# Performance work log

Hardware: AMD Instinct MI355X
Metric: run time of the kernel (lower is better)

## Reference

```python
import jax, jax.numpy as jnp
import numpy as np

N_NODES = 50000
N_EDGES = 600000
N_RELS = 19
D_IN = 128
D_HID = 64
D_OUT = 2


def setup_inputs() -> dict:
    key = jax.random.key(0)
    ks = jax.random.split(key, 10)
    feat = jax.random.normal(ks[0], (N_NODES, D_IN), dtype=jnp.float32)
    src = jax.random.randint(ks[1], (N_EDGES,), 0, N_NODES)
    dst = jax.random.randint(ks[2], (N_EDGES,), 0, N_NODES)
    etype = jax.random.randint(ks[3], (N_EDGES,), 0, N_RELS)
    s1 = 1.0 / np.sqrt(D_IN)
    s2 = 1.0 / np.sqrt(D_HID)
    W1 = jax.random.normal(ks[4], (N_RELS, D_IN, D_HID), dtype=jnp.float32) * s1
    loop1 = jax.random.normal(ks[5], (D_IN, D_HID), dtype=jnp.float32) * s1
    b1 = jnp.zeros((D_HID,), dtype=jnp.float32)
    W2 = jax.random.normal(ks[6], (N_RELS, D_HID, D_OUT), dtype=jnp.float32) * s2
    loop2 = jax.random.normal(ks[7], (D_HID, D_OUT), dtype=jnp.float32) * s2
    b2 = jnp.zeros((D_OUT,), dtype=jnp.float32)
    return {"feat": feat, "W1": W1, "loop1": loop1, "b1": b1,
            "W2": W2, "loop2": loop2, "b2": b2,
            "src": src, "dst": dst, "etype": etype}


def _rel_graph_conv(h, W, loop_w, bias, src, dst, etype, activation):
    # Per-relation transform of all nodes: [N, R, O]; then gather per edge.
    # (num_rels * out_feat is small, so this is cheaper than gathering W per edge.)
    transformed = jnp.einsum('nd,rdo->nro', h, W)
    msg = transformed[src, etype]                      # [E, O] edge messages
    agg = jax.ops.segment_sum(msg, dst, num_segments=h.shape[0])  # scatter-add
    out = agg + h @ loop_w + bias                      # self-loop + bias
    if activation is not None:
        out = activation(out)
    return out


def reference(feat, W1, loop1, b1, W2, loop2, b2, src, dst, etype):
    h = _rel_graph_conv(feat, W1, loop1, b1, src, dst, etype, jax.nn.relu)
    h = _rel_graph_conv(h, W2, loop2, b2, src, dst, etype, None)
    return h
```

## Files before the change

kernel.cpp:

```cpp
#include <hip/hip_runtime.h>

#define N_NODES 50000
#define N_EDGES 600000
#define N_RELS  19
#define D_IN    128
#define D_HID   64
#define D_OUT   2

typedef unsigned short u16;
typedef unsigned int   u32;
typedef __attribute__((ext_vector_type(8))) short sfrag;
typedef __attribute__((ext_vector_type(4))) float f32x4;

__device__ __forceinline__ u16 f2bf(float f){
  union { float f; u32 i; } v; v.f = f;
  u32 r = v.i + 0x7fffu + ((v.i >> 16) & 1u);
  return (u16)(r >> 16);
}
__device__ __forceinline__ float bf2f(u16 u){
  union { u32 i; float f; } v; v.i = ((u32)u) << 16; return v.f;
}

__global__ __launch_bounds__(256) void k_featb(const float* __restrict__ feat,
                                               u16* __restrict__ featb){
  int i = blockIdx.x * 256 + threadIdx.x;
  float2 f = ((const float2*)feat)[i];
  ((u32*)featb)[i] = (u32)f2bf(f.x) | ((u32)f2bf(f.y) << 16);
}

__global__ void k_prep(const float* __restrict__ W1, const float* __restrict__ loop1,
                       const float* __restrict__ W2,
                       u16* __restrict__ W1Tb, u16* __restrict__ loop1Tb,
                       u16* __restrict__ W2Tb){
  int idx = blockIdx.x * 256 + threadIdx.x;
  const int T1 = N_RELS * D_HID * D_IN;
  const int T2 = T1 + N_RELS * 16 * D_HID;
  const int T3 = T2 + D_HID * D_IN;
  if (idx < T1) {
    int r = idx / (D_HID * D_IN);
    int t = idx - r * (D_HID * D_IN);
    int j = t >> 7, d = t & 127;
    W1Tb[idx] = f2bf(W1[(r * D_IN + d) * D_HID + j]);
  } else if (idx < T2) {
    int k2 = idx - T1;
    int r = k2 / (16 * D_HID);
    int t = k2 - r * (16 * D_HID);
    int n = t >> 6, k = t & 63;
    W2Tb[k2] = (n < D_OUT) ? f2bf(W2[(r * D_HID + k) * D_OUT + n]) : (u16)0;
  } else if (idx < T3) {
    int k2 = idx - T2;
    int j = k2 >> 7, d = k2 & 127;
    loop1Tb[k2] = f2bf(loop1[d * D_HID + j]);
  }
}

__global__ void k_zero(int* __restrict__ hist){
  if (threadIdx.x < N_RELS) hist[threadIdx.x] = 0;
}

__global__ __launch_bounds__(256) void k_hist(const int* __restrict__ et, int* __restrict__ hist){
  __shared__ int lh[N_RELS];
  int tid = threadIdx.x;
  if (tid < N_RELS) lh[tid] = 0;
  __syncthreads();
  int e = blockIdx.x * 256 + tid;
  if (e < N_EDGES) atomicAdd(&lh[et[e]], 1);
  __syncthreads();
  if (tid < N_RELS && lh[tid]) atomicAdd(&hist[tid], lh[tid]);
}

__global__ void k_scan(const int* __restrict__ hist, int* __restrict__ offs,
                       int* __restrict__ toff, int* __restrict__ cursor){
  if (threadIdx.x == 0) {
    int acc = 0, tacc = 0;
    offs[0] = 0; toff[0] = 0;
    for (int r = 0; r < N_RELS; ++r) {
      cursor[r] = acc;
      int c = hist[r];
      acc += c;               offs[r + 1] = acc;
      tacc += (c + 63) >> 6;  toff[r + 1] = tacc;
    }
  }
}

__global__ __launch_bounds__(256) void k_scatter(const int* __restrict__ et,
                                                 int* __restrict__ cursor,
                                                 int* __restrict__ perm){
  __shared__ int lh[N_RELS], base[N_RELS];
  int tid = threadIdx.x;
  if (tid < N_RELS) lh[tid] = 0;
  __syncthreads();
  int e = blockIdx.x * 256 + tid;
  int r = 0, my = 0;
  bool valid = e < N_EDGES;
  if (valid) { r = et[e]; my = atomicAdd(&lh[r], 1); }
  __syncthreads();
  if (tid < N_RELS && lh[tid]) base[tid] = atomicAdd(&cursor[tid], lh[tid]);
  __syncthreads();
  if (valid) perm[base[r] + my] = e;
}

__global__ __launch_bounds__(256) void k_selfloop1_mfma(
    const u16* __restrict__ featb, const u16* __restrict__ loop1Tb,
    const float* __restrict__ b1, u16* __restrict__ agg1b){
  __shared__ __align__(16) u16 Als[64][136];
  __shared__ __align__(16) u16 Bls[64][136];
  int tid = threadIdx.x;
  int base = blockIdx.x * 64;
  {
    int j = tid >> 2, seg = tid & 3;
    const uint4* g = (const uint4*)(loop1Tb + j * 128) + seg * 4;
    uint4* d = (uint4*)&Bls[j][seg * 32];
    d[0] = g[0]; d[1] = g[1]; d[2] = g[2]; d[3] = g[3];
  }
  {
    int i = tid >> 2, seg = tid & 3;
    int n = base + i; if (n >= N_NODES) n = N_NODES - 1;
    const uint4* g = (const uint4*)(featb + n * D_IN) + seg * 4;
    uint4* d = (uint4*)&Als[i][seg * 32];
    d[0] = g[0]; d[1] = g[1]; d[2] = g[2]; d[3] = g[3];
  }
  __syncthreads();

  int w = tid >> 6, lane = tid & 63;
  int r16 = lane & 15, c4 = lane >> 4;
  sfrag aF[4];
  #pragma unroll
  for (int kk = 0; kk < 4; ++kk)
    aF[kk] = *(const sfrag*)&Als[w * 16 + r16][kk * 32 + c4 * 8];
  #pragma unroll
  for (int ct = 0; ct < 4; ++ct) {
    f32x4 acc = {0.f, 0.f, 0.f, 0.f};
    #pragma unroll
    for (int kk = 0; kk < 4; ++kk) {
      sfrag bF = *(const sfrag*)&Bls[ct * 16 + r16][kk * 32 + c4 * 8];
      acc = __builtin_amdgcn_mfma_f32_16x16x32_bf16(aF[kk], bF, acc, 0, 0, 0);
    }
    int col = ct * 16 + r16;
    float bias = b1[col];
    #pragma unroll
    for (int reg = 0; reg < 4; ++reg) {
      int row = base + w * 16 + c4 * 4 + reg;
      if (row < N_NODES) agg1b[row * D_HID + col] = f2bf(acc[reg] + bias);
    }
  }
}

__global__ __launch_bounds__(256) void k_edge1_mfma(
    const u16* __restrict__ featb, const u16* __restrict__ W1Tb,
    const int* __restrict__ src, const int* __restrict__ dst,
    const int* __restrict__ perm, const int* __restrict__ offs,
    const int* __restrict__ toff, u16* __restrict__ agg1b){
  __shared__ __align__(16) u16 Als[64][136];
  __shared__ __align__(16) u16 Bls[64][136];
  __shared__ int dstIds[64];
  __shared__ int sMeta[3];
  int tid = threadIdx.x;
  if (tid == 0) {
    int b = blockIdx.x, r = 0, vc = 0, ts = 0;
    if (b < toff[N_RELS]) {
      while (b >= toff[r + 1]) ++r;
      ts = offs[r] + ((b - toff[r]) << 6);
      vc = offs[r + 1] - ts; if (vc > 64) vc = 64;
    }
    sMeta[0] = r; sMeta[1] = ts; sMeta[2] = vc;
  }
  __syncthreads();
  int vcount = sMeta[2];
  if (vcount == 0) return;
  int rel = sMeta[0], tileStart = sMeta[1];

  {
    int j = tid >> 2, seg = tid & 3;
    const uint4* g = (const uint4*)(W1Tb + (rel * 64 + j) * 128) + seg * 4;
    uint4* d = (uint4*)&Bls[j][seg * 32];
    d[0] = g[0]; d[1] = g[1]; d[2] = g[2]; d[3] = g[3];
  }
  {
    int i = tid >> 2, seg = tid & 3;
    if (i < vcount) {
      int e = perm[tileStart + i];
      if (seg == 0) dstIds[i] = dst[e];
      const uint4* g = (const uint4*)(featb + src[e] * D_IN) + seg * 4;
      uint4* d = (uint4*)&Als[i][seg * 32];
      d[0] = g[0]; d[1] = g[1]; d[2] = g[2]; d[3] = g[3];
    } else {
      if (seg == 0) dstIds[i] = -1;
      uint4 z = make_uint4(0, 0, 0, 0);
      uint4* d = (uint4*)&Als[i][seg * 32];
      d[0] = z; d[1] = z; d[2] = z; d[3] = z;
    }
  }
  __syncthreads();

  int w = tid >> 6, lane = tid & 63;
  int r16 = lane & 15, c4 = lane >> 4;
  sfrag aF[4];
  #pragma unroll
  for (int kk = 0; kk < 4; ++kk)
    aF[kk] = *(const sfrag*)&Als[w * 16 + r16][kk * 32 + c4 * 8];
  #pragma unroll
  for (int ct = 0; ct < 4; ++ct) {
    f32x4 acc = {0.f, 0.f, 0.f, 0.f};
    #pragma unroll
    for (int kk = 0; kk < 4; ++kk) {
      sfrag bF = *(const sfrag*)&Bls[ct * 16 + r16][kk * 32 + c4 * 8];
      acc = __builtin_amdgcn_mfma_f32_16x16x32_bf16(aF[kk], bF, acc, 0, 0, 0);
    }
    int col = ct * 16 + r16;
    #pragma unroll
    for (int reg = 0; reg < 4; ++reg) {
      float other = __shfl_xor(acc[reg], 1);
      if (!(r16 & 1)) {
        int row = w * 16 + c4 * 4 + reg;
        int dn = dstIds[row];
        if (dn >= 0) {
          u32 p = (u32)f2bf(acc[reg]) | ((u32)f2bf(other) << 16);
          unsigned long long a = (unsigned long long)(agg1b + dn * D_HID + col);
          asm volatile("global_atomic_pk_add_bf16 %0, %1, off"
                       :: "v"(a), "v"(p) : "memory");
        }
      }
    }
  }
  asm volatile("s_waitcnt vmcnt(0)" ::: "memory");
}

__global__ __launch_bounds__(256) void k_relu_self2(u16* __restrict__ agg1b,
                                                     const float* __restrict__ loop2,
                                                     const float* __restrict__ b2,
                                                     float* __restrict__ out){
  int wave = threadIdx.x >> 6, lane = threadIdx.x & 63;
  int n = blockIdx.x * 4 + wave;
  u16 u = agg1b[n * D_HID + lane];
  float v = bf2f(u);
  bool neg = v <= 0.f;
  if (neg) v = 0.f;
  agg1b[n * D_HID + lane] = neg ? (u16)0 : u;
  float2 lw = ((const float2*)loop2)[lane];
  float p0 = v * lw.x, p1 = v * lw.y;
  for (int off = 32; off; off >>= 1) {
    p0 += __shfl_down(p0, off);
    p1 += __shfl_down(p1, off);
  }
  if (lane == 0) {
    out[n * 2]     = p0 + b2[0];
    out[n * 2 + 1] = p1 + b2[1];
  }
}

__global__ __launch_bounds__(256) void k_edge2_mfma(
    const u16* __restrict__ h1b, const u16* __restrict__ W2Tb,
    const int* __restrict__ src, const int* __restrict__ dst,
    const int* __restrict__ perm, const int* __restrict__ offs,
    const int* __restrict__ toff, float* __restrict__ out){
  __shared__ __align__(16) u16 Als[64][72];
  __shared__ __align__(16) u16 Bls[16][72];
  __shared__ int dstIds[64];
  __shared__ int sMeta[3];
  int tid = threadIdx.x;
  if (tid == 0) {
    int b = blockIdx.x, r = 0, vc = 0, ts = 0;
    if (b < toff[N_RELS]) {
      while (b >= toff[r + 1]) ++r;
      ts = offs[r] + ((b - toff[r]) << 6);
      vc = offs[r + 1] - ts; if (vc > 64) vc = 64;
    }
    sMeta[0] = r; sMeta[1] = ts; sMeta[2] = vc;
  }
  __syncthreads();
  int vcount = sMeta[2];
  if (vcount == 0) return;
  int rel = sMeta[0], tileStart = sMeta[1];

  if (tid < 128) {
    int n = tid >> 3, q = tid & 7;
    ((uint4*)&Bls[n][0])[q] = ((const uint4*)(W2Tb + rel * 16 * 64))[tid];
  }
  {
    int i = tid >> 2, seg = tid & 3;
    if (i < vcount) {
      int e = perm[tileStart + i];
      if (seg == 0) dstIds[i] = dst[e];
      const uint4* g = (const uint4*)(h1b + src[e] * D_HID) + seg * 2;
      *(uint4*)&Als[i][seg * 16]     = g[0];
      *(uint4*)&Als[i][seg * 16 + 8] = g[1];
    } else {
      if (seg == 0) dstIds[i] = -1;
      uint4 z = make_uint4(0, 0, 0, 0);
      *(uint4*)&Als[i][seg * 16]     = z;
      *(uint4*)&Als[i][seg * 16 + 8] = z;
    }
  }
  __syncthreads();

  int w = tid >> 6, lane = tid & 63;
  int r16 = lane & 15, c4 = lane >> 4;
  f32x4 acc = {0.f, 0.f, 0.f, 0.f};
  #pragma unroll
  for (int kk = 0; kk < 2; ++kk) {
    sfrag aF = *(const sfrag*)&Als[w * 16 + r16][kk * 32 + c4 * 8];
    sfrag bF = *(const sfrag*)&Bls[r16][kk * 32 + c4 * 8];
    acc = __builtin_amdgcn_mfma_f32_16x16x32_bf16(aF, bF, acc, 0, 0, 0);
  }
  if (r16 < D_OUT) {
    #pragma unroll
    for (int reg = 0; reg < 4; ++reg) {
      int row = w * 16 + c4 * 4 + reg;
      int dn = dstIds[row];
      if (dn >= 0) atomicAdd(&out[dn * D_OUT + r16], acc[reg]);
    }
  }
}

extern "C" void kernel_launch(void* const* d_in, const int* in_sizes, int n_in,
                              void* d_out, int out_size, void* d_ws, size_t ws_size,
                              hipStream_t stream){
  const float* feat  = (const float*)d_in[0];
  const float* W1    = (const float*)d_in[1];
  const float* loop1 = (const float*)d_in[2];
  const float* b1    = (const float*)d_in[3];
  const float* W2    = (const float*)d_in[4];
  const float* loop2 = (const float*)d_in[5];
  const float* b2    = (const float*)d_in[6];
  const int* src     = (const int*)d_in[7];
  const int* dst     = (const int*)d_in[8];
  const int* et      = (const int*)d_in[9];
  float* out = (float*)d_out;

  char* w = (char*)d_ws;
  u16*   W1Tb    = (u16*)(w);
  u16*   W2Tb    = (u16*)(w + 311296);
  u16*   loop1Tb = (u16*)(w + 350208);
  int*   hist    = (int*)(w + 382976);
  int*   cursor  = (int*)(w + 383104);
  int*   offs    = (int*)(w + 383232);
  int*   toff    = (int*)(w + 383360);
  int*   perm    = (int*)(w + 383488);
  u16*   featb   = (u16*)(w + 2783488);
  u16*   agg1b   = (u16*)(w + 15583488);

  const int MAX_TILES = (N_EDGES + 63) / 64 + N_RELS;

  k_prep          <<<716,   256, 0, stream>>>(W1, loop1, W2, W1Tb, loop1Tb, W2Tb);
  k_featb         <<<12500, 256, 0, stream>>>(feat, featb);
  k_zero          <<<1,      64, 0, stream>>>(hist);
  k_hist          <<<2344,  256, 0, stream>>>(et, hist);
  k_scan          <<<1,      64, 0, stream>>>(hist, offs, toff, cursor);
  k_scatter       <<<2344,  256, 0, stream>>>(et, cursor, perm);
  k_selfloop1_mfma<<<(N_NODES + 63) / 64, 256, 0, stream>>>(featb, loop1Tb, b1, agg1b);
  k_edge1_mfma    <<<MAX_TILES,   256, 0, stream>>>(featb, W1Tb, src, dst, perm, offs, toff, agg1b);
  k_relu_self2    <<<N_NODES / 4, 256, 0, stream>>>(agg1b, loop2, b2, out);
  k_edge2_mfma    <<<MAX_TILES,   256, 0, stream>>>(agg1b, W2Tb, src, dst, perm, offs, toff, out);
}
```

Before: 336.2 us.

## Replace layer-1 bf16 atomic scatter with dst-CSR message buffer and segmented reduction

Builds a destination histogram and prefix scan so that each edge message from the layer-1 relation GEMM is written to a slot grouped by destination, instead of being atomically added into the bf16 aggregate. A new per-node kernel sums each node's messages, adds the fp32 self-loop term and applies ReLU. Edge tiles grow to 128 rows and relation lookup uses a wave ballot. The aim is to remove atomic contention and bf16 accumulation on agg1; the cost is extra preprocessing kernels, a serial single-block scan, per-edge atomics on the cursor, and a 77 MB message buffer round-trip.

```diff
diff --git a/kernel.cpp b/kernel.cpp
--- a/kernel.cpp
+++ b/kernel.cpp
@@ -54,11 +54,14 @@
   }
 }
 
-__global__ void k_zero(int* __restrict__ hist){
-  if (threadIdx.x < N_RELS) hist[threadIdx.x] = 0;
-}
-
-__global__ __launch_bounds__(256) void k_hist(const int* __restrict__ et, int* __restrict__ hist){
+__global__ __launch_bounds__(256) void k_zero_all(int* __restrict__ hist_rel,
+                                                  int* __restrict__ hist_dst){
+  int i = blockIdx.x * 256 + threadIdx.x;
+  if (i < N_NODES) hist_dst[i] = 0;
+  if (i < N_RELS)  hist_rel[i] = 0;
+}
+
+__global__ __launch_bounds__(256) void k_hist_rel(const int* __restrict__ et, int* __restrict__ hist){
   __shared__ int lh[N_RELS];
   int tid = threadIdx.x;
   if (tid < N_RELS) lh[tid] = 0;
@@ -69,23 +72,51 @@
   if (tid < N_RELS && lh[tid]) atomicAdd(&hist[tid], lh[tid]);
 }
 
-__global__ void k_scan(const int* __restrict__ hist, int* __restrict__ offs,
-                       int* __restrict__ toff, int* __restrict__ cursor){
+__global__ __launch_bounds__(256) void k_hist_dst(const int* __restrict__ dst, int* __restrict__ hist){
+  int e = blockIdx.x * 256 + threadIdx.x;
+  if (e < N_EDGES) atomicAdd(&hist[dst[e]], 1);
+}
+
+__global__ void k_scan_rel(const int* __restrict__ hist, int* __restrict__ offs,
+                           int* __restrict__ toff, int* __restrict__ cursor){
   if (threadIdx.x == 0) {
     int acc = 0, tacc = 0;
     offs[0] = 0; toff[0] = 0;
     for (int r = 0; r < N_RELS; ++r) {
       cursor[r] = acc;
       int c = hist[r];
-      acc += c;               offs[r + 1] = acc;
-      tacc += (c + 63) >> 6;  toff[r + 1] = tacc;
-    }
-  }
-}
-
-__global__ __launch_bounds__(256) void k_scatter(const int* __restrict__ et,
-                                                 int* __restrict__ cursor,
-                                                 int* __restrict__ perm){
+      acc += c;                offs[r + 1] = acc;
+      tacc += (c + 127) >> 7;  toff[r + 1] = tacc;
+    }
+  }
+}
+
+__global__ __launch_bounds__(256) void k_scan_dst(const int* __restrict__ hist,
+                                                  int* __restrict__ dcsr,
+                                                  int* __restrict__ cursor){
+  __shared__ int wsum[4];
+  int tid = threadIdx.x, lane = tid & 63, w = tid >> 6;
+  const int CH = 196;
+  int start = tid * CH;
+  int s = 0;
+  for (int i = 0; i < CH; ++i) { int idx = start + i; if (idx < N_NODES) s += hist[idx]; }
+  int v = s;
+  for (int o = 1; o < 64; o <<= 1) { int u = __shfl_up(v, o); if (lane >= o) v += u; }
+  if (lane == 63) wsum[w] = v;
+  __syncthreads();
+  int woff = 0;
+  for (int i = 0; i < w; ++i) woff += wsum[i];
+  int run = woff + v - s;
+  for (int i = 0; i < CH; ++i) {
+    int idx = start + i;
+    if (idx < N_NODES) { dcsr[idx] = run; cursor[idx] = run; run += hist[idx]; }
+  }
+  if (tid == 255) dcsr[N_NODES] = run;
+}
+
+__global__ __launch_bounds__(256) void k_scatter_rel(const int* __restrict__ et,
+                                                     int* __restrict__ cursor,
+                                                     int* __restrict__ perm){
   __shared__ int lh[N_RELS], base[N_RELS];
   int tid = threadIdx.x;
   if (tid < N_RELS) lh[tid] = 0;
@@ -102,24 +133,20 @@
 
 __global__ __launch_bounds__(256) void k_selfloop1_mfma(
     const u16* __restrict__ featb, const u16* __restrict__ loop1Tb,
-    const float* __restrict__ b1, u16* __restrict__ agg1b){
+    const float* __restrict__ b1, float* __restrict__ agg1f){
   __shared__ __align__(16) u16 Als[64][136];
   __shared__ __align__(16) u16 Bls[64][136];
   int tid = threadIdx.x;
   int base = blockIdx.x * 64;
-  {
-    int j = tid >> 2, seg = tid & 3;
+  { int j = tid >> 2, seg = tid & 3;
     const uint4* g = (const uint4*)(loop1Tb + j * 128) + seg * 4;
     uint4* d = (uint4*)&Bls[j][seg * 32];
-    d[0] = g[0]; d[1] = g[1]; d[2] = g[2]; d[3] = g[3];
-  }
-  {
-    int i = tid >> 2, seg = tid & 3;
+    d[0] = g[0]; d[1] = g[1]; d[2] = g[2]; d[3] = g[3]; }
+  { int i = tid >> 2, seg = tid & 3;
     int n = base + i; if (n >= N_NODES) n = N_NODES - 1;
-    const uint4* g = (const uint4*)(featb + n * D_IN) + seg * 4;
+    const uint4* g = (const uint4*)(featb + (size_t)n * D_IN) + seg * 4;
     uint4* d = (uint4*)&Als[i][seg * 32];
-    d[0] = g[0]; d[1] = g[1]; d[2] = g[2]; d[3] = g[3];
-  }
+    d[0] = g[0]; d[1] = g[1]; d[2] = g[2]; d[3] = g[3]; }
   __syncthreads();
 
   int w = tid >> 6, lane = tid & 63;
@@ -141,7 +168,7 @@
     #pragma unroll
     for (int reg = 0; reg < 4; ++reg) {
       int row = base + w * 16 + c4 * 4 + reg;
-      if (row < N_NODES) agg1b[row * D_HID + col] = f2bf(acc[reg] + bias);
+      if (row < N_NODES) agg1f[(size_t)row * D_HID + col] = acc[reg] + bias;
     }
   }
 }
@@ -150,95 +177,130 @@
     const u16* __restrict__ featb, const u16* __restrict__ W1Tb,
     const int* __restrict__ src, const int* __restrict__ dst,
     const int* __restrict__ perm, const int* __restrict__ offs,
-    const int* __restrict__ toff, u16* __restrict__ agg1b){
-  __shared__ __align__(16) u16 Als[64][136];
+    const int* __restrict__ toff, const int* __restrict__ dcsr,
+    int* __restrict__ cursor, u16* __restrict__ msgbuf){
+  __shared__ __align__(16) u16 Als[128][136];
   __shared__ __align__(16) u16 Bls[64][136];
-  __shared__ int dstIds[64];
-  __shared__ int sMeta[3];
-  int tid = threadIdx.x;
-  if (tid == 0) {
-    int b = blockIdx.x, r = 0, vc = 0, ts = 0;
-    if (b < toff[N_RELS]) {
-      while (b >= toff[r + 1]) ++r;
-      ts = offs[r] + ((b - toff[r]) << 6);
-      vc = offs[r + 1] - ts; if (vc > 64) vc = 64;
-    }
-    sMeta[0] = r; sMeta[1] = ts; sMeta[2] = vc;
-  }
-  __syncthreads();
-  int vcount = sMeta[2];
-  if (vcount == 0) return;
-  int rel = sMeta[0], tileStart = sMeta[1];
+  __shared__ int posIds[128];
+  int tid = threadIdx.x, lane = tid & 63, w = tid >> 6;
+
+  int b = blockIdx.x;
+  unsigned long long mm = __ballot((lane < N_RELS) && (b >= toff[lane + 1]));
+  int rel = __popcll(mm);
+  if (rel >= N_RELS) return;
+  int ts = offs[rel] + ((b - toff[rel]) << 7);
+  int vc = offs[rel + 1] - ts; if (vc > 128) vc = 128;
 
   {
     int j = tid >> 2, seg = tid & 3;
-    const uint4* g = (const uint4*)(W1Tb + (rel * 64 + j) * 128) + seg * 4;
+    const uint4* g = (const uint4*)(W1Tb + ((size_t)rel * 64 + j) * 128) + seg * 4;
     uint4* d = (uint4*)&Bls[j][seg * 32];
     d[0] = g[0]; d[1] = g[1]; d[2] = g[2]; d[3] = g[3];
   }
-  {
-    int i = tid >> 2, seg = tid & 3;
-    if (i < vcount) {
-      int e = perm[tileStart + i];
-      if (seg == 0) dstIds[i] = dst[e];
-      const uint4* g = (const uint4*)(featb + src[e] * D_IN) + seg * 4;
+  #pragma unroll
+  for (int p = 0; p < 2; ++p) {
+    int i = p * 64 + (tid >> 2), seg = tid & 3;
+    if (i < vc) {
+      int e = perm[ts + i];
+      if (seg == 0) posIds[i] = atomicAdd(&cursor[dst[e]], 1);
+      const uint4* g = (const uint4*)(featb + (size_t)src[e] * D_IN) + seg * 4;
       uint4* d = (uint4*)&Als[i][seg * 32];
       d[0] = g[0]; d[1] = g[1]; d[2] = g[2]; d[3] = g[3];
-    } else {
-      if (seg == 0) dstIds[i] = -1;
-      uint4 z = make_uint4(0, 0, 0, 0);
-      uint4* d = (uint4*)&Als[i][seg * 32];
-      d[0] = z; d[1] = z; d[2] = z; d[3] = z;
-    }
-  }
-  __syncthreads();
-
-  int w = tid >> 6, lane = tid & 63;
+    } else if (seg == 0) posIds[i] = -1;
+  }
+  __syncthreads();
+
   int r16 = lane & 15, c4 = lane >> 4;
-  sfrag aF[4];
-  #pragma unroll
-  for (int kk = 0; kk < 4; ++kk)
-    aF[kk] = *(const sfrag*)&Als[w * 16 + r16][kk * 32 + c4 * 8];
+  sfrag aF[2][4];
+  #pragma unroll
+  for (int mt = 0; mt < 2; ++mt)
+    #pragma unroll
+    for (int kk = 0; kk < 4; ++kk)
+      aF[mt][kk] = *(const sfrag*)&Als[w * 32 + mt * 16 + r16][kk * 32 + c4 * 8];
+  f32x4 accAll[2][4];
   #pragma unroll
   for (int ct = 0; ct < 4; ++ct) {
-    f32x4 acc = {0.f, 0.f, 0.f, 0.f};
-    #pragma unroll
-    for (int kk = 0; kk < 4; ++kk) {
-      sfrag bF = *(const sfrag*)&Bls[ct * 16 + r16][kk * 32 + c4 * 8];
-      acc = __builtin_amdgcn_mfma_f32_16x16x32_bf16(aF[kk], bF, acc, 0, 0, 0);
-    }
-    int col = ct * 16 + r16;
-    #pragma unroll
-    for (int reg = 0; reg < 4; ++reg) {
-      float other = __shfl_xor(acc[reg], 1);
-      if (!(r16 & 1)) {
-        int row = w * 16 + c4 * 4 + reg;
-        int dn = dstIds[row];
-        if (dn >= 0) {
-          u32 p = (u32)f2bf(acc[reg]) | ((u32)f2bf(other) << 16);
-          unsigned long long a = (unsigned long long)(agg1b + dn * D_HID + col);
-          asm volatile("global_atomic_pk_add_bf16 %0, %1, off"
-                       :: "v"(a), "v"(p) : "memory");
-        }
+    sfrag bF[4];
+    #pragma unroll
+    for (int kk = 0; kk < 4; ++kk)
+      bF[kk] = *(const sfrag*)&Bls[ct * 16 + r16][kk * 32 + c4 * 8];
+    #pragma unroll
+    for (int mt = 0; mt < 2; ++mt) {
+      f32x4 acc = {0.f, 0.f, 0.f, 0.f};
+      #pragma unroll
+      for (int kk = 0; kk < 4; ++kk)
+        acc = __builtin_amdgcn_mfma_f32_16x16x32_bf16(aF[mt][kk], bF[kk], acc, 0, 0, 0);
+      accAll[mt][ct] = acc;
+    }
+  }
+  float* msg = (float*)&Als[0][0];
+  #pragma unroll
+  for (int mt = 0; mt < 2; ++mt)
+    #pragma unroll
+    for (int ct = 0; ct < 4; ++ct) {
+      int col = ct * 16 + r16;
+      #pragma unroll
+      for (int reg = 0; reg < 4; ++reg) {
+        int row = w * 32 + mt * 16 + c4 * 4 + reg;
+        msg[row * 68 + col] = accAll[mt][ct][reg];
       }
     }
-  }
-  asm volatile("s_waitcnt vmcnt(0)" ::: "memory");
-}
-
-__global__ __launch_bounds__(256) void k_relu_self2(u16* __restrict__ agg1b,
-                                                     const float* __restrict__ loop2,
-                                                     const float* __restrict__ b2,
-                                                     float* __restrict__ out){
-  int wave = threadIdx.x >> 6, lane = threadIdx.x & 63;
-  int n = blockIdx.x * 4 + wave;
-  u16 u = agg1b[n * D_HID + lane];
-  float v = bf2f(u);
-  bool neg = v <= 0.f;
-  if (neg) v = 0.f;
-  agg1b[n * D_HID + lane] = neg ? (u16)0 : u;
-  float2 lw = ((const float2*)loop2)[lane];
-  float p0 = v * lw.x, p1 = v * lw.y;
+  __syncthreads();
+  { int row = tid >> 1, half = tid & 1;
+    int pos = posIds[row];
+    if (pos >= 0) {
+      const float* mr = msg + row * 68 + half * 32;
+      u32 pk[16];
+      #pragma unroll
+      for (int q = 0; q < 16; ++q)
+        pk[q] = (u32)f2bf(mr[2 * q]) | ((u32)f2bf(mr[2 * q + 1]) << 16);
+      uint4* d = (uint4*)(msgbuf + (size_t)pos * D_HID + half * 32);
+      d[0] = *(uint4*)&pk[0];  d[1] = *(uint4*)&pk[4];
+      d[2] = *(uint4*)&pk[8];  d[3] = *(uint4*)&pk[12];
+    } }
+}
+
+__global__ __launch_bounds__(256) void k_agg(const u16* __restrict__ msgbuf,
+                                             const int* __restrict__ dcsr,
+                                             const float* __restrict__ agg1f,
+                                             u16* __restrict__ h1b){
+  int wv = threadIdx.x >> 6, lane = threadIdx.x & 63;
+  int n = blockIdx.x * 4 + wv;
+  int s = dcsr[n], epos = dcsr[n + 1];
+  int h = lane >> 5, c = lane & 31;
+  float a0 = 0.f, a1 = 0.f;
+  for (int i = s + h; i < epos; i += 2) {
+    u32 v = ((const u32*)msgbuf)[(size_t)i * 32 + c];
+    a0 += bf2f((u16)(v & 0xffffu));
+    a1 += bf2f((u16)(v >> 16));
+  }
+  a0 += __shfl_down(a0, 32);
+  a1 += __shfl_down(a1, 32);
+  if (h == 0) {
+    float2 sl = ((const float2*)(agg1f + (size_t)n * D_HID))[c];
+    float v0 = a0 + sl.x, v1 = a1 + sl.y;
+    v0 = v0 > 0.f ? v0 : 0.f;
+    v1 = v1 > 0.f ? v1 : 0.f;
+    ((u32*)h1b)[n * 32 + c] = (u32)f2bf(v0) | ((u32)f2bf(v1) << 16);
+  }
+}
+
+__global__ __launch_bounds__(256) void k_self2(const u16* __restrict__ h1b,
+                                               const float* __restrict__ loop2,
+                                               const float* __restrict__ b2,
+                                               float* __restrict__ out){
+  int wv = threadIdx.x >> 6, lane = threadIdx.x & 63;
+  int n = blockIdx.x * 4 + wv;
+  float p0 = 0.f, p1 = 0.f;
+  if (lane < 32) {
+    u32 v = ((const u32*)h1b)[n * 32 + lane];
+    float h0 = bf2f((u16)(v & 0xffffu));
+    float h1v = bf2f((u16)(v >> 16));
+    float2 w0 = ((const float2*)loop2)[2 * lane];
+    float2 w1 = ((const float2*)loop2)[2 * lane + 1];
+    p0 = h0 * w0.x + h1v * w1.x;
+    p1 = h0 * w0.y + h1v * w1.y;
+  }
   for (int off = 32; off; off >>= 1) {
     p0 += __shfl_down(p0, off);
     p1 += __shfl_down(p1, off);
@@ -254,61 +316,50 @@
     const int* __restrict__ src, const int* __restrict__ dst,
     const int* __restrict__ perm, const int* __restrict__ offs,
     const int* __restrict__ toff, float* __restrict__ out){
-  __shared__ __align__(16) u16 Als[64][72];
+  __shared__ __align__(16) u16 Als[128][72];
   __shared__ __align__(16) u16 Bls[16][72];
-  __shared__ int dstIds[64];
-  __shared__ int sMeta[3];
-  int tid = threadIdx.x;
-  if (tid == 0) {
-    int b = blockIdx.x, r = 0, vc = 0, ts = 0;
-    if (b < toff[N_RELS]) {
-      while (b >= toff[r + 1]) ++r;
-      ts = offs[r] + ((b - toff[r]) << 6);
-      vc = offs[r + 1] - ts; if (vc > 64) vc = 64;
-    }
-    sMeta[0] = r; sMeta[1] = ts; sMeta[2] = vc;
-  }
-  __syncthreads();
-  int vcount = sMeta[2];
-  if (vcount == 0) return;
-  int rel = sMeta[0], tileStart = sMeta[1];
+  __shared__ int dstIds[128];
+  int tid = threadIdx.x, lane = tid & 63, w = tid >> 6;
+
+  int b = blockIdx.x;
+  unsigned long long mm = __ballot((lane < N_RELS) && (b >= toff[lane + 1]));
+  int rel = __popcll(mm);
+  if (rel >= N_RELS) return;
+  int ts = offs[rel] + ((b - toff[rel]) << 7);
+  int vc = offs[rel + 1] - ts; if (vc > 128) vc = 128;
 
   if (tid < 128) {
-    int n = tid >> 3, q = tid & 7;
-    ((uint4*)&Bls[n][0])[q] = ((const uint4*)(W2Tb + rel * 16 * 64))[tid];
+    ((uint4*)&Bls[tid >> 3][0])[tid & 7] = ((const uint4*)(W2Tb + (size_t)rel * 16 * 64))[tid];
   }
   {
-    int i = tid >> 2, seg = tid & 3;
-    if (i < vcount) {
-      int e = perm[tileStart + i];
-      if (seg == 0) dstIds[i] = dst[e];
-      const uint4* g = (const uint4*)(h1b + src[e] * D_HID) + seg * 2;
-      *(uint4*)&Als[i][seg * 16]     = g[0];
-      *(uint4*)&Als[i][seg * 16 + 8] = g[1];
-    } else {
-      if (seg == 0) dstIds[i] = -1;
-      uint4 z = make_uint4(0, 0, 0, 0);
-      *(uint4*)&Als[i][seg * 16]     = z;
-      *(uint4*)&Als[i][seg * 16 + 8] = z;
-    }
-  }
-  __syncthreads();
-
-  int w = tid >> 6, lane = tid & 63;
+    int i = tid >> 1, half = tid & 1;
+    if (i < vc) {
+      int e = perm[ts + i];
+      if (half == 0) dstIds[i] = dst[e];
+      const uint4* g = (const uint4*)(h1b + (size_t)src[e] * D_HID) + half * 4;
+      uint4* d = (uint4*)&Als[i][half * 32];
+      d[0] = g[0]; d[1] = g[1]; d[2] = g[2]; d[3] = g[3];
+    } else if (half == 0) dstIds[i] = -1;
+  }
+  __syncthreads();
+
   int r16 = lane & 15, c4 = lane >> 4;
-  f32x4 acc = {0.f, 0.f, 0.f, 0.f};
-  #pragma unroll
-  for (int kk = 0; kk < 2; ++kk) {
-    sfrag aF = *(const sfrag*)&Als[w * 16 + r16][kk * 32 + c4 * 8];
-    sfrag bF = *(const sfrag*)&Bls[r16][kk * 32 + c4 * 8];
-    acc = __builtin_amdgcn_mfma_f32_16x16x32_bf16(aF, bF, acc, 0, 0, 0);
-  }
-  if (r16 < D_OUT) {
-    #pragma unroll
-    for (int reg = 0; reg < 4; ++reg) {
-      int row = w * 16 + c4 * 4 + reg;
-      int dn = dstIds[row];
-      if (dn >= 0) atomicAdd(&out[dn * D_OUT + r16], acc[reg]);
+  #pragma unroll
+  for (int mt = 0; mt < 2; ++mt) {
+    f32x4 acc = {0.f, 0.f, 0.f, 0.f};
+    #pragma unroll
+    for (int kk = 0; kk < 2; ++kk) {
+      sfrag aF = *(const sfrag*)&Als[w * 32 + mt * 16 + r16][kk * 32 + c4 * 8];
+      sfrag bF = *(const sfrag*)&Bls[r16][kk * 32 + c4 * 8];
+      acc = __builtin_amdgcn_mfma_f32_16x16x32_bf16(aF, bF, acc, 0, 0, 0);
+    }
+    if (r16 < D_OUT) {
+      #pragma unroll
+      for (int reg = 0; reg < 4; ++reg) {
+        int row = w * 32 + mt * 16 + c4 * 4 + reg;
+        int dn = dstIds[row];
+        if (dn >= 0) atomicAdd(&out[dn * D_OUT + r16], acc[reg]);
+      }
     }
   }
 }
@@ -329,27 +380,36 @@
   float* out = (float*)d_out;
 
   char* w = (char*)d_ws;
-  u16*   W1Tb    = (u16*)(w);
-  u16*   W2Tb    = (u16*)(w + 311296);
-  u16*   loop1Tb = (u16*)(w + 350208);
-  int*   hist    = (int*)(w + 382976);
-  int*   cursor  = (int*)(w + 383104);
-  int*   offs    = (int*)(w + 383232);
-  int*   toff    = (int*)(w + 383360);
-  int*   perm    = (int*)(w + 383488);
-  u16*   featb   = (u16*)(w + 2783488);
-  u16*   agg1b   = (u16*)(w + 15583488);
-
-  const int MAX_TILES = (N_EDGES + 63) / 64 + N_RELS;
+  u16*   W1Tb     = (u16*)(w);
+  u16*   W2Tb     = (u16*)(w + 311296);
+  u16*   loop1Tb  = (u16*)(w + 350208);
+  int*   hist_rel = (int*)(w + 366592);
+  int*   offs     = (int*)(w + 366720);
+  int*   toff     = (int*)(w + 366848);
+  int*   cur_rel  = (int*)(w + 366976);
+  int*   hist_dst = (int*)(w + 367104);
+  int*   dcsr     = (int*)(w + 567104);
+  int*   cur_dst  = (int*)(w + 767120);
+  int*   perm     = (int*)(w + 967120);
+  u16*   featb    = (u16*)(w + 3367120);
+  float* agg1f    = (float*)(w + 16167120);
+  u16*   h1b      = (u16*)(w + 28967120);
+  u16*   msgbuf   = (u16*)(w + 35367120);
+
+  const int MAX_TILES = (N_EDGES + 127) / 128 + N_RELS;
 
   k_prep          <<<716,   256, 0, stream>>>(W1, loop1, W2, W1Tb, loop1Tb, W2Tb);
   k_featb         <<<12500, 256, 0, stream>>>(feat, featb);
-  k_zero          <<<1,      64, 0, stream>>>(hist);
-  k_hist          <<<2344,  256, 0, stream>>>(et, hist);
-  k_scan          <<<1,      64, 0, stream>>>(hist, offs, toff, cursor);
-  k_scatter       <<<2344,  256, 0, stream>>>(et, cursor, perm);
-  k_selfloop1_mfma<<<(N_NODES + 63) / 64, 256, 0, stream>>>(featb, loop1Tb, b1, agg1b);
-  k_edge1_mfma    <<<MAX_TILES,   256, 0, stream>>>(featb, W1Tb, src, dst, perm, offs, toff, agg1b);
-  k_relu_self2    <<<N_NODES / 4, 256, 0, stream>>>(agg1b, loop2, b2, out);
-  k_edge2_mfma    <<<MAX_TILES,   256, 0, stream>>>(agg1b, W2Tb, src, dst, perm, offs, toff, out);
-}
+  k_zero_all      <<<196,   256, 0, stream>>>(hist_rel, hist_dst);
+  k_hist_rel      <<<2344,  256, 0, stream>>>(et, hist_rel);
+  k_hist_dst      <<<2344,  256, 0, stream>>>(dst, hist_dst);
+  k_scan_rel      <<<1,      64, 0, stream>>>(hist_rel, offs, toff, cur_rel);
+  k_scan_dst      <<<1,     256, 0, stream>>>(hist_dst, dcsr, cur_dst);
+  k_scatter_rel   <<<2344,  256, 0, stream>>>(et, cur_rel, perm);
+  k_selfloop1_mfma<<<(N_NODES + 63) / 64, 256, 0, stream>>>(featb, loop1Tb, b1, agg1f);
+  k_edge1_mfma    <<<MAX_TILES, 256, 0, stream>>>(featb, W1Tb, src, dst, perm, offs, toff,
+                                                  dcsr, cur_dst, msgbuf);
+  k_agg           <<<12500, 256, 0, stream>>>(msgbuf, dcsr, agg1f, h1b);
+  k_self2         <<<12500, 256, 0, stream>>>(h1b, loop2, b2, out);
+  k_edge2_mfma    <<<MAX_TILES, 256, 0, stream>>>(h1b, W2Tb, src, dst, perm, offs, toff, out);
+}
```

New measurement: 477.8 us. +42.1%, slower.
